# Kernel tuning notes

Hardware: AMD Instinct MI355X
Metric: run time of the kernel (lower is better)

The kernel has to match this reference:

```python
import jax, jax.numpy as jnp
import numpy as np

B, M, N, I, O, NM = 16, 256, 256, 64, 64, 16


def setup_inputs() -> dict:
    key = jax.random.key(0)
    k1, k2, k3, k4, k5 = jax.random.split(key, 5)
    glorot = 1.0 / np.sqrt(I + O)
    return {
        "x": jax.random.normal(k1, (B, M, N, I), dtype=jnp.float32),
        "fw1": jax.random.normal(k2, (I, O, NM, NM, 2), dtype=jnp.float32) * glorot,
        "fw2": jax.random.normal(k3, (I, O, NM, NM, 2), dtype=jnp.float32) * glorot,
        "W": jax.random.normal(k4, (I, O), dtype=jnp.float32) * glorot,
        "b": jnp.zeros((O,), dtype=jnp.float32),
    }


def reference(x, fw1, fw2, W, b):
    # x: [B, M, N, I] -> [B, I, M, N]
    Bs, Ms, Ns, Is = x.shape
    nm = fw1.shape[2]
    xt = jnp.transpose(x, (0, 3, 1, 2))
    # forward rFFT over spatial dims, scaled by 1/sqrt(M*N) as in the TF code
    x_ft = jnp.fft.rfft2(xt, s=(Ms, Ns))  # [B, I, M, N//2+1] complex64
    x_ft = x_ft / jnp.asarray(np.sqrt(Ms * Ns), dtype=x_ft.dtype)
    # complex weights (stack-of-2 real/imag -> complex); complex einsum is
    # exactly the real/imag stacked matmul in the original
    w1 = jax.lax.complex(fw1[..., 0], fw1[..., 1])
    w2 = jax.lax.complex(fw2[..., 0], fw2[..., 1])
    top = jnp.einsum('bixy,ioxy->boxy', x_ft[:, :, :nm, :nm], w1)
    bot = jnp.einsum('bixy,ioxy->boxy', x_ft[:, :, -nm:, :nm], w2)
    mid = jnp.zeros((Bs, top.shape[1], Ms - 2 * nm, nm), dtype=top.dtype)
    out_ft = jnp.concatenate([top, mid, bot], axis=2)          # [B, O, M, nm]
    pad = jnp.zeros((Bs, top.shape[1], Ms, Ms // 2 + 1 - nm), dtype=top.dtype)
    out_ft = jnp.concatenate([out_ft, pad], axis=3)            # [B, O, M, M//2+1]
    y = jnp.fft.irfft2(out_ft, s=(Ns, Ms))                     # [B, O, N, M]
    # TF rescale: sqrt(prod of last two dims of out_ft) = sqrt(N*(M//2+1))
    y = y * jnp.asarray(np.sqrt(Ns * (Ms // 2 + 1)), dtype=y.dtype)
    y = jnp.transpose(y, (0, 2, 3, 1))                         # [B, M, N, O]
    return jax.nn.relu(y @ W + b + y)
```

## Files before the change

kernel.cpp:

```cpp
#include <hip/hip_runtime.h>
#include <hip/hip_bf16.h>


#define PI2F 6.283185307179586f

typedef __attribute__((ext_vector_type(8))) short short8v;
typedef __attribute__((ext_vector_type(4))) float f32x4;

static __device__ __forceinline__ unsigned short f_to_bf16(float f) {
  unsigned int u = __float_as_uint(f);
  u += 0x7fffu + ((u >> 16) & 1u);
  return (unsigned short)(u >> 16);
}
static __device__ __forceinline__ unsigned int pack_bf16(float lo, float hi) {
  return (unsigned int)f_to_bf16(lo) | ((unsigned int)f_to_bf16(hi) << 16);
}

__global__ __launch_bounds__(256) void k_prep(const float* __restrict__ fw1,
                                              const float* __restrict__ fw2,
                                              float2* __restrict__ wT,
                                              unsigned short* __restrict__ Eg,
                                              unsigned short* __restrict__ CSg,
                                              const float* __restrict__ Wg,
                                              unsigned short* __restrict__ Wtb) {
  int t = threadIdx.x;
  if (blockIdx.x == 256) {
#pragma unroll
    for (int ky = 0; ky < 16; ++ky) {
      int idx = (ky * t) & 255;
      float ss, cc;
      sincosf(PI2F * (float)idx * (1.0f / 256.0f), &ss, &cc);
      Eg[(2 * ky) * 256 + t]     = f_to_bf16(cc);
      Eg[(2 * ky + 1) * 256 + t] = f_to_bf16(-ss);
      CSg[t * 32 + 2 * ky]       = f_to_bf16(cc);
      CSg[t * 32 + 2 * ky + 1]   = f_to_bf16(ss);
    }
#pragma unroll
    for (int k = 0; k < 16; ++k) {
      int p = k * 256 + t;
      Wtb[(p & 63) * 64 + (p >> 6)] = f_to_bf16(Wg[p]);
    }
    return;
  }
  int a  = blockIdx.x >> 3;
  int ic = blockIdx.x & 7;
  const float* w = (a < 16) ? fw1 : fw2;
  int xx = a & 15;
#pragma unroll
  for (int k = 0; k < 2; ++k) {
    int p = k * 256 + t;
    int i = ic * 8 + (p >> 6);
    int o = p & 63;
    const float4* s4 = reinterpret_cast<const float4*>(
        w + ((((size_t)i * 64 + o) * 16 + xx) * 16) * 2);
#pragma unroll
    for (int j = 0; j < 8; ++j) {
      float4 q = s4[j];
      wT[(((size_t)(2 * j) * 32 + a) * 64 + i) * 64 + o]     = make_float2(q.x, q.y);
      wT[(((size_t)(2 * j + 1) * 32 + a) * 64 + i) * 64 + o] = make_float2(q.z, q.w);
    }
  }
}

__global__ __launch_bounds__(256) void k1_mfma(const float* __restrict__ x,
                                               const unsigned short* __restrict__ Eg,
                                               unsigned int* __restrict__ Tb) {
  __shared__ __align__(16) unsigned short El[32 * 264];
  __shared__ __align__(16) float xs[2][2048];
  int bm = blockIdx.x;
  int b = bm >> 8, m = bm & 255;
  int tid = threadIdx.x;

  {
    const unsigned int* src = reinterpret_cast<const unsigned int*>(Eg);
    unsigned int* dst = reinterpret_cast<unsigned int*>(El);
#pragma unroll
    for (int t = 0; t < 16; ++t) {
      int idx = t * 256 + tid;
      dst[(idx >> 7) * 132 + (idx & 127)] = src[idx];
    }
  }

  const float* xrow = x + (size_t)bm * 16384;
  int lane = tid & 63, w = tid >> 6;
  int r16 = lane & 15, g4 = lane >> 4;

  {
    const float4* s = reinterpret_cast<const float4*>(xrow);
    float4 v0 = s[tid], v1 = s[256 + tid];
    float4* d = reinterpret_cast<float4*>(xs[0]);
    d[tid] = v0;
    d[256 + tid] = v1;
  }
  __syncthreads();

  f32x4 z = {0.f, 0.f, 0.f, 0.f};
  f32x4 acc0 = z, acc1 = z;

#pragma unroll
  for (int c = 0; c < 8; ++c) {
    int cur = c & 1;
    if (c < 7) {
      const float4* s = reinterpret_cast<const float4*>(xrow + (c + 1) * 2048);
      float4 v0 = s[tid], v1 = s[256 + tid];
      float4* d = reinterpret_cast<float4*>(xs[cur ^ 1]);
      d[tid] = v0;
      d[256 + tid] = v1;
    }
    const float* xb = &xs[cur][g4 * 8 * 64 + (w * 16 + r16)];
    float xv[8];
#pragma unroll
    for (int j = 0; j < 8; ++j) xv[j] = xb[j * 64];
    short8v bfr;
#pragma unroll
    for (int j = 0; j < 8; ++j) bfr[j] = (short)f_to_bf16(xv[j]);
    int nb = c * 32 + g4 * 8;
    short8v a0 = *reinterpret_cast<const short8v*>(&El[r16 * 264 + nb]);
    short8v a1 = *reinterpret_cast<const short8v*>(&El[(16 + r16) * 264 + nb]);
    acc0 = __builtin_amdgcn_mfma_f32_16x16x32_bf16(a0, bfr, acc0, 0, 0, 0);
    acc1 = __builtin_amdgcn_mfma_f32_16x16x32_bf16(a1, bfr, acc1, 0, 0, 0);
    __syncthreads();
  }

  const float SC = 1.0f / 256.0f;
  int i = w * 16 + r16;
#pragma unroll
  for (int mt = 0; mt < 2; ++mt) {
    f32x4 av = (mt == 0) ? acc0 : acc1;
    int ky_a = mt * 8 + g4 * 2;
    Tb[((size_t)(b * 16 + ky_a) * 256 + m) * 64 + i]     = pack_bf16(av[0] * SC, av[1] * SC);
    Tb[((size_t)(b * 16 + ky_a + 1) * 256 + m) * 64 + i] = pack_bf16(av[2] * SC, av[3] * SC);
  }
}

__global__ __launch_bounds__(256) void k2_fwd_m(const unsigned int* __restrict__ Tb,
                                                float* __restrict__ Xp) {
  int bx = blockIdx.x;
  int bky = bx & 255, mc = bx >> 8;
  int m0 = mc * 64;
  int ih = threadIdx.x & 15;
  int ag = threadIdx.x >> 4;
  const uint4* Tp4 = reinterpret_cast<const uint4*>(Tb) + (size_t)bky * 4096 + ih;

  float cd1, sd1n, cd2, sd2n;
  { float ss, cc; sincosf(PI2F * (float)ag * (1.0f / 256.0f), &ss, &cc); cd1 = cc; sd1n = -ss; }
  { float ss, cc; sincosf(PI2F * (float)(ag - 16) * (1.0f / 256.0f), &ss, &cc); cd2 = cc; sd2n = -ss; }
  float c1, s1, c2, s2;
  { int t = (ag * m0) & 255; float ss, cc; sincosf(PI2F * (float)t * (1.0f / 256.0f), &ss, &cc); c1 = cc; s1 = -ss; }
  { int t = ((ag + 240) * m0) & 255; float ss, cc; sincosf(PI2F * (float)t * (1.0f / 256.0f), &ss, &cc); c2 = cc; s2 = -ss; }

  float xr1[4], xi1[4], xr2[4], xi2[4];
#pragma unroll
  for (int ii = 0; ii < 4; ++ii) { xr1[ii] = xi1[ii] = xr2[ii] = xi2[ii] = 0.0f; }

#pragma unroll 4
  for (int m = 0; m < 64; ++m) {
    uint4 q = Tp4[(size_t)(m0 + m) * 16];
    unsigned int dv[4] = {q.x, q.y, q.z, q.w};
    float tre[4], tim[4];
#pragma unroll
    for (int ii = 0; ii < 4; ++ii) {
      tre[ii] = __uint_as_float(dv[ii] << 16);
      tim[ii] = __uint_as_float(dv[ii] & 0xffff0000u);
    }
#pragma unroll
    for (int ii = 0; ii < 4; ++ii) {
      xr1[ii] += tre[ii] * c1 - tim[ii] * s1;
      xi1[ii] += tre[ii] * s1 + tim[ii] * c1;
      xr2[ii] += tre[ii] * c2 - tim[ii] * s2;
      xi2[ii] += tre[ii] * s2 + tim[ii] * c2;
    }
    float cn;
    cn = c1 * cd1 - s1 * sd1n; s1 = c1 * sd1n + s1 * cd1; c1 = cn;
    cn = c2 * cd2 - s2 * sd2n; s2 = c2 * sd2n + s2 * cd2; c2 = cn;
  }

  float* Xb = Xp + (size_t)mc * 1048576;
  float* Xp1 = Xb + ((size_t)bky * 32 + ag) * 128 + ih * 8;
  float* Xp2 = Xb + ((size_t)bky * 32 + ag + 16) * 128 + ih * 8;
  reinterpret_cast<float4*>(Xp1)[0] = make_float4(xr1[0], xi1[0], xr1[1], xi1[1]);
  reinterpret_cast<float4*>(Xp1)[1] = make_float4(xr1[2], xi1[2], xr1[3], xi1[3]);
  reinterpret_cast<float4*>(Xp2)[0] = make_float4(xr2[0], xi2[0], xr2[1], xi2[1]);
  reinterpret_cast<float4*>(Xp2)[1] = make_float4(xr2[2], xi2[2], xr2[3], xi2[3]);
}

__global__ __launch_bounds__(256) void k3_mix(const float* __restrict__ Xp,
                                              const float* __restrict__ wT,
                                              float* __restrict__ OF) {
  int blk = blockIdx.x;
  int kyy = blk >> 5, a = blk & 31;
  __shared__ float wre[64 * 65];
  __shared__ float wim[64 * 65];
  __shared__ float xsh[16 * 128];

  const float2* wsrc = reinterpret_cast<const float2*>(wT) + (size_t)(kyy * 32 + a) * 4096;
#pragma unroll
  for (int k = 0; k < 16; ++k) {
    int p = k * 256 + (int)threadIdx.x;
    float2 v = wsrc[p];
    int i = p >> 6, o = p & 63;
    wre[i * 65 + o] = v.x;
    wim[i * 65 + o] = v.y;
  }
  {
    int bb = threadIdx.x >> 4, icn = threadIdx.x & 15;
    size_t off = ((size_t)(bb * 16 + kyy) * 32 + a) * 128;
    float4 a0 = make_float4(0.f, 0.f, 0.f, 0.f), a1 = a0;
#pragma unroll
    for (int c = 0; c < 4; ++c) {
      const float4* xsrc = reinterpret_cast<const float4*>(Xp + (size_t)c * 1048576 + off);
      float4 q0 = xsrc[icn * 2], q1 = xsrc[icn * 2 + 1];
      a0.x += q0.x; a0.y += q0.y; a0.z += q0.z; a0.w += q0.w;
      a1.x += q1.x; a1.y += q1.y; a1.z += q1.z; a1.w += q1.w;
    }
    float4* xdst = reinterpret_cast<float4*>(xsh + bb * 128);
    xdst[icn * 2]     = a0;
    xdst[icn * 2 + 1] = a1;
  }
  __syncthreads();

  int o = threadIdx.x & 63, bg = threadIdx.x >> 6;
#pragma unroll
  for (int bb = 0; bb < 4; ++bb) {
    int b = bg * 4 + bb;
    float ore = 0.0f, oim = 0.0f;
    for (int i = 0; i < 64; ++i) {
      float xr = xsh[b * 128 + 2 * i], xi = xsh[b * 128 + 2 * i + 1];
      float wr = wre[i * 65 + o],     wi = wim[i * 65 + o];
      ore += xr * wr - xi * wi;
      oim += xr * wi + xi * wr;
    }
    reinterpret_cast<float2*>(OF)[(((size_t)b * 16 + kyy) * 32 + a) * 64 + o] =
        make_float2(ore, oim);
  }
}

__global__ __launch_bounds__(256) void k4_inv_kx(const float* __restrict__ OF,
                                                 uint4* __restrict__ Gb4) {
  int bx = blockIdx.x;
  int b = bx >> 6, ug = (bx >> 2) & 15, chunk = bx & 3;
  __shared__ float ofs[16384];
  __shared__ float ct[256], st[256];
  {
    float ssv, ccv;
    sincosf(PI2F * (float)threadIdx.x * (1.0f / 256.0f), &ssv, &ccv);
    ct[threadIdx.x] = ccv;
    st[threadIdx.x] = ssv;
  }
  {
    const float4* src = reinterpret_cast<const float4*>(
        OF + ((size_t)b * 16 + chunk * 4) * 4096);
    float4* dst = reinterpret_cast<float4*>(ofs);
#pragma unroll
    for (int k = 0; k < 16; ++k) dst[k * 256 + threadIdx.x] = src[k * 256 + threadIdx.x];
  }
  __syncthreads();

  int o = threadIdx.x & 63, us = threadIdx.x >> 6;
  int u0 = ug * 16 + us * 4;
  const float SC2 = 0.002772904280510622f;

  float accr[4][4], acci[4][4];
#pragma unroll
  for (int du = 0; du < 4; ++du)
#pragma unroll
    for (int kyl = 0; kyl < 4; ++kyl) { accr[du][kyl] = 0.0f; acci[du][kyl] = 0.0f; }

  for (int a = 0; a < 32; ++a) {
    int kx = (a < 16) ? a : (224 + a);
    float ofr[4], ofi[4];
#pragma unroll
    for (int kyl = 0; kyl < 4; ++kyl) {
      ofr[kyl] = ofs[((kyl * 32 + a) * 64 + o) * 2];
      ofi[kyl] = ofs[((kyl * 32 + a) * 64 + o) * 2 + 1];
    }
#pragma unroll
    for (int du = 0; du < 4; ++du) {
      int t = (kx * (u0 + du)) & 255;
      float cv = ct[t], sv = st[t];
#pragma unroll
      for (int kyl = 0; kyl < 4; ++kyl) {
        accr[du][kyl] += ofr[kyl] * cv - ofi[kyl] * sv;
        acci[du][kyl] += ofr[kyl] * sv + ofi[kyl] * cv;
      }
    }
  }
#pragma unroll
  for (int du = 0; du < 4; ++du) {
    int u = u0 + du;
    unsigned int wv[4];
#pragma unroll
    for (int kyl = 0; kyl < 4; ++kyl) {
      int ky = chunk * 4 + kyl;
      float sc = SC2 * ((ky == 0) ? 1.0f : 2.0f);
      wv[kyl] = pack_bf16(accr[du][kyl] * sc, -acci[du][kyl] * sc);
    }
    uint4 pk; pk.x = wv[0]; pk.y = wv[1]; pk.z = wv[2]; pk.w = wv[3];
    Gb4[(((size_t)b * 256 + u) * 64 + o) * 4 + chunk] = pk;
  }
}

__global__ __launch_bounds__(256) void k5_mfma(const unsigned short* __restrict__ Gb,
                                               const unsigned short* __restrict__ CSg,
                                               const unsigned short* __restrict__ Wtb,
                                               const float* __restrict__ bias,
                                               float* __restrict__ out) {
  __shared__ __align__(16) unsigned short yl[256 * 72];

  int blk = blockIdx.x;
  int tid = threadIdx.x;
  int lane = tid & 63, w = tid >> 6;
  int r16 = lane & 15, g4 = lane >> 4;
  int kc0 = g4 * 8;

  f32x4 z = {0.f, 0.f, 0.f, 0.f};
  f32x4 acc[4][4];

  short8v af[4], bfx[4];
#pragma unroll
  for (int vt = 0; vt < 4; ++vt)
    af[vt] = *reinterpret_cast<const short8v*>(&CSg[(w * 64 + vt * 16 + r16) * 32 + kc0]);
#pragma unroll
  for (int ot = 0; ot < 4; ++ot)
    bfx[ot] = *reinterpret_cast<const short8v*>(
        &Gb[((size_t)blk * 64 + ot * 16 + r16) * 32 + kc0]);
#pragma unroll
  for (int vt = 0; vt < 4; ++vt)
#pragma unroll
    for (int ot = 0; ot < 4; ++ot)
      acc[vt][ot] = __builtin_amdgcn_mfma_f32_16x16x32_bf16(af[vt], bfx[ot], z, 0, 0, 0);

#pragma unroll
  for (int vt = 0; vt < 4; ++vt)
#pragma unroll
    for (int ot = 0; ot < 4; ++ot)
#pragma unroll
      for (int r = 0; r < 4; ++r)
        yl[(w * 64 + vt * 16 + g4 * 4 + r) * 72 + ot * 16 + r16] = f_to_bf16(acc[vt][ot][r]);

#pragma unroll
  for (int ot = 0; ot < 4; ++ot) {
    float bv = bias[ot * 16 + r16];
#pragma unroll
    for (int vt = 0; vt < 4; ++vt)
#pragma unroll
      for (int r = 0; r < 4; ++r) acc[vt][ot][r] += bv;
  }

#pragma unroll
  for (int ks = 0; ks < 2; ++ks) {
    int k0 = ks * 32 + kc0;
    short8v ya[4], wb[4];
#pragma unroll
    for (int vt = 0; vt < 4; ++vt)
      ya[vt] = *reinterpret_cast<const short8v*>(&yl[(w * 64 + vt * 16 + r16) * 72 + k0]);
#pragma unroll
    for (int ot = 0; ot < 4; ++ot)
      wb[ot] = *reinterpret_cast<const short8v*>(&Wtb[(ot * 16 + r16) * 64 + k0]);
#pragma unroll
    for (int vt = 0; vt < 4; ++vt)
#pragma unroll
      for (int ot = 0; ot < 4; ++ot)
        acc[vt][ot] = __builtin_amdgcn_mfma_f32_16x16x32_bf16(ya[vt], wb[ot], acc[vt][ot], 0, 0, 0);
  }

  float* ob = out + (size_t)blk * 16384;
  float* tw = reinterpret_cast<float*>(&yl[w * 4608]);
#pragma unroll
  for (int vt = 0; vt < 4; ++vt) {
#pragma unroll
    for (int ot = 0; ot < 4; ++ot)
#pragma unroll
      for (int r = 0; r < 4; ++r)
        tw[(g4 * 4 + r) * 68 + ot * 16 + r16] = fmaxf(acc[vt][ot][r], 0.0f);
    float* obase = ob + (size_t)(w * 64 + vt * 16) * 64;
#pragma unroll
    for (int q = 0; q < 4; ++q) {
      float4 vv = *reinterpret_cast<const float4*>(
          &tw[(q * 4 + (lane >> 4)) * 68 + (lane & 15) * 4]);
      *reinterpret_cast<float4*>(&obase[q * 256 + lane * 4]) = vv;
    }
  }
}

extern "C" void kernel_launch(void* const* d_in, const int* in_sizes, int n_in,
                              void* d_out, int out_size, void* d_ws, size_t ws_size,
                              hipStream_t stream) {
  const float* x   = (const float*)d_in[0];
  const float* fw1 = (const float*)d_in[1];
  const float* fw2 = (const float*)d_in[2];
  const float* W   = (const float*)d_in[3];
  const float* bb  = (const float*)d_in[4];
  float* out = (float*)d_out;

  float* ws = (float*)d_ws;
  float* wT          = ws;
  unsigned int* Tb   = (unsigned int*)(ws + 4194304);
  float* Xp          = ws + 8388608;
  float* OF          = ws + 12582912;
  unsigned int* Gb   = (unsigned int*)(ws + 13631488);
  unsigned short* Eg  = (unsigned short*)(ws + 17825792);
  unsigned short* CSg = Eg + 8192;
  unsigned short* Wtb = CSg + 8192;

  hipLaunchKernelGGL(k_prep,   dim3(257),  dim3(256), 0, stream,
                     fw1, fw2, (float2*)wT, Eg, CSg, W, Wtb);
  hipLaunchKernelGGL(k1_mfma,  dim3(4096), dim3(256), 0, stream, x, Eg, Tb);
  hipLaunchKernelGGL(k2_fwd_m, dim3(1024), dim3(256), 0, stream, Tb, Xp);
  hipLaunchKernelGGL(k3_mix,   dim3(512),  dim3(256), 0, stream, Xp, wT, OF);
  hipLaunchKernelGGL(k4_inv_kx,dim3(1024), dim3(256), 0, stream, OF, (uint4*)Gb);
  hipLaunchKernelGGL(k5_mfma,  dim3(4096), dim3(256), 0, stream,
                     (const unsigned short*)Gb, CSg, Wtb, bb, out);
}
```

Baseline: 233.6 us.

## Read spectral weights directly in mixing kernel and split inverse kx work finer

The weight transpose pass in the prep kernel is removed, so the mixing kernel now gathers complex weights straight from fw1/fw2 with strided float2 loads, and the prep kernel shrinks to a single block for twiddle and W tables. This drops a 16 MB write and re-read of a transposed weight copy, at the cost of uncoalesced 8-byte reads (stride 128 bytes) in the mixing kernel. Separately, the inverse-kx kernel now processes 2 ky values per block instead of 4, doubling the grid to 2048 blocks and halving shared memory per block for better occupancy. It writes 8-byte packed pairs instead of 16-byte ones.

```diff
diff --git a/kernel.cpp b/kernel.cpp
--- a/kernel.cpp
+++ b/kernel.cpp
@@ -16,49 +16,25 @@
   return (unsigned int)f_to_bf16(lo) | ((unsigned int)f_to_bf16(hi) << 16);
 }
 
-__global__ __launch_bounds__(256) void k_prep(const float* __restrict__ fw1,
-                                              const float* __restrict__ fw2,
-                                              float2* __restrict__ wT,
-                                              unsigned short* __restrict__ Eg,
-                                              unsigned short* __restrict__ CSg,
-                                              const float* __restrict__ Wg,
-                                              unsigned short* __restrict__ Wtb) {
+__global__ __launch_bounds__(256) void k_prep1(unsigned short* __restrict__ Eg,
+                                               unsigned short* __restrict__ CSg,
+                                               const float* __restrict__ Wg,
+                                               unsigned short* __restrict__ Wtb) {
   int t = threadIdx.x;
-  if (blockIdx.x == 256) {
-#pragma unroll
-    for (int ky = 0; ky < 16; ++ky) {
-      int idx = (ky * t) & 255;
-      float ss, cc;
-      sincosf(PI2F * (float)idx * (1.0f / 256.0f), &ss, &cc);
-      Eg[(2 * ky) * 256 + t]     = f_to_bf16(cc);
-      Eg[(2 * ky + 1) * 256 + t] = f_to_bf16(-ss);
-      CSg[t * 32 + 2 * ky]       = f_to_bf16(cc);
-      CSg[t * 32 + 2 * ky + 1]   = f_to_bf16(ss);
-    }
-#pragma unroll
-    for (int k = 0; k < 16; ++k) {
-      int p = k * 256 + t;
-      Wtb[(p & 63) * 64 + (p >> 6)] = f_to_bf16(Wg[p]);
-    }
-    return;
-  }
-  int a  = blockIdx.x >> 3;
-  int ic = blockIdx.x & 7;
-  const float* w = (a < 16) ? fw1 : fw2;
-  int xx = a & 15;
-#pragma unroll
-  for (int k = 0; k < 2; ++k) {
+#pragma unroll
+  for (int ky = 0; ky < 16; ++ky) {
+    int idx = (ky * t) & 255;
+    float ss, cc;
+    sincosf(PI2F * (float)idx * (1.0f / 256.0f), &ss, &cc);
+    Eg[(2 * ky) * 256 + t]     = f_to_bf16(cc);
+    Eg[(2 * ky + 1) * 256 + t] = f_to_bf16(-ss);
+    CSg[t * 32 + 2 * ky]       = f_to_bf16(cc);
+    CSg[t * 32 + 2 * ky + 1]   = f_to_bf16(ss);
+  }
+#pragma unroll
+  for (int k = 0; k < 16; ++k) {
     int p = k * 256 + t;
-    int i = ic * 8 + (p >> 6);
-    int o = p & 63;
-    const float4* s4 = reinterpret_cast<const float4*>(
-        w + ((((size_t)i * 64 + o) * 16 + xx) * 16) * 2);
-#pragma unroll
-    for (int j = 0; j < 8; ++j) {
-      float4 q = s4[j];
-      wT[(((size_t)(2 * j) * 32 + a) * 64 + i) * 64 + o]     = make_float2(q.x, q.y);
-      wT[(((size_t)(2 * j + 1) * 32 + a) * 64 + i) * 64 + o] = make_float2(q.z, q.w);
-    }
+    Wtb[(p & 63) * 64 + (p >> 6)] = f_to_bf16(Wg[p]);
   }
 }
 
@@ -185,7 +161,8 @@
 }
 
 __global__ __launch_bounds__(256) void k3_mix(const float* __restrict__ Xp,
-                                              const float* __restrict__ wT,
+                                              const float* __restrict__ fw1,
+                                              const float* __restrict__ fw2,
                                               float* __restrict__ OF) {
   int blk = blockIdx.x;
   int kyy = blk >> 5, a = blk & 31;
@@ -193,11 +170,12 @@
   __shared__ float wim[64 * 65];
   __shared__ float xsh[16 * 128];
 
-  const float2* wsrc = reinterpret_cast<const float2*>(wT) + (size_t)(kyy * 32 + a) * 4096;
+  const float* w = (a < 16) ? fw1 : fw2;
+  int xx = a & 15;
 #pragma unroll
   for (int k = 0; k < 16; ++k) {
     int p = k * 256 + (int)threadIdx.x;
-    float2 v = wsrc[p];
+    float2 v = *reinterpret_cast<const float2*>(w + ((size_t)p * 16 + xx) * 32 + kyy * 2);
     int i = p >> 6, o = p & 63;
     wre[i * 65 + o] = v.x;
     wim[i * 65 + o] = v.y;
@@ -236,10 +214,10 @@
 }
 
 __global__ __launch_bounds__(256) void k4_inv_kx(const float* __restrict__ OF,
-                                                 uint4* __restrict__ Gb4) {
+                                                 unsigned int* __restrict__ Gbd) {
   int bx = blockIdx.x;
-  int b = bx >> 6, ug = (bx >> 2) & 15, chunk = bx & 3;
-  __shared__ float ofs[16384];
+  int b = bx >> 7, ug = (bx >> 3) & 15, kyc = bx & 7;
+  __shared__ float ofs[8192];
   __shared__ float ct[256], st[256];
   {
     float ssv, ccv;
@@ -249,10 +227,10 @@
   }
   {
     const float4* src = reinterpret_cast<const float4*>(
-        OF + ((size_t)b * 16 + chunk * 4) * 4096);
+        OF + ((size_t)b * 16 + kyc * 2) * 4096);
     float4* dst = reinterpret_cast<float4*>(ofs);
 #pragma unroll
-    for (int k = 0; k < 16; ++k) dst[k * 256 + threadIdx.x] = src[k * 256 + threadIdx.x];
+    for (int k = 0; k < 8; ++k) dst[k * 256 + threadIdx.x] = src[k * 256 + threadIdx.x];
   }
   __syncthreads();
 
@@ -260,17 +238,17 @@
   int u0 = ug * 16 + us * 4;
   const float SC2 = 0.002772904280510622f;
 
-  float accr[4][4], acci[4][4];
+  float accr[4][2], acci[4][2];
 #pragma unroll
   for (int du = 0; du < 4; ++du)
 #pragma unroll
-    for (int kyl = 0; kyl < 4; ++kyl) { accr[du][kyl] = 0.0f; acci[du][kyl] = 0.0f; }
+    for (int kyl = 0; kyl < 2; ++kyl) { accr[du][kyl] = 0.0f; acci[du][kyl] = 0.0f; }
 
   for (int a = 0; a < 32; ++a) {
     int kx = (a < 16) ? a : (224 + a);
-    float ofr[4], ofi[4];
-#pragma unroll
-    for (int kyl = 0; kyl < 4; ++kyl) {
+    float ofr[2], ofi[2];
+#pragma unroll
+    for (int kyl = 0; kyl < 2; ++kyl) {
       ofr[kyl] = ofs[((kyl * 32 + a) * 64 + o) * 2];
       ofi[kyl] = ofs[((kyl * 32 + a) * 64 + o) * 2 + 1];
     }
@@ -279,7 +257,7 @@
       int t = (kx * (u0 + du)) & 255;
       float cv = ct[t], sv = st[t];
 #pragma unroll
-      for (int kyl = 0; kyl < 4; ++kyl) {
+      for (int kyl = 0; kyl < 2; ++kyl) {
         accr[du][kyl] += ofr[kyl] * cv - ofi[kyl] * sv;
         acci[du][kyl] += ofr[kyl] * sv + ofi[kyl] * cv;
       }
@@ -288,15 +266,16 @@
 #pragma unroll
   for (int du = 0; du < 4; ++du) {
     int u = u0 + du;
-    unsigned int wv[4];
-#pragma unroll
-    for (int kyl = 0; kyl < 4; ++kyl) {
-      int ky = chunk * 4 + kyl;
+    unsigned int wv[2];
+#pragma unroll
+    for (int kyl = 0; kyl < 2; ++kyl) {
+      int ky = kyc * 2 + kyl;
       float sc = SC2 * ((ky == 0) ? 1.0f : 2.0f);
       wv[kyl] = pack_bf16(accr[du][kyl] * sc, -acci[du][kyl] * sc);
     }
-    uint4 pk; pk.x = wv[0]; pk.y = wv[1]; pk.z = wv[2]; pk.w = wv[3];
-    Gb4[(((size_t)b * 256 + u) * 64 + o) * 4 + chunk] = pk;
+    uint2 pk; pk.x = wv[0]; pk.y = wv[1];
+    *reinterpret_cast<uint2*>(
+        &Gbd[(((size_t)b * 256 + u) * 64 + o) * 16 + kyc * 2]) = pk;
   }
 }
 
@@ -394,7 +373,6 @@
   float* out = (float*)d_out;
 
   float* ws = (float*)d_ws;
-  float* wT          = ws;
   unsigned int* Tb   = (unsigned int*)(ws + 4194304);
   float* Xp          = ws + 8388608;
   float* OF          = ws + 12582912;
@@ -403,12 +381,11 @@
   unsigned short* CSg = Eg + 8192;
   unsigned short* Wtb = CSg + 8192;
 
-  hipLaunchKernelGGL(k_prep,   dim3(257),  dim3(256), 0, stream,
-                     fw1, fw2, (float2*)wT, Eg, CSg, W, Wtb);
+  hipLaunchKernelGGL(k_prep1,  dim3(1),    dim3(256), 0, stream, Eg, CSg, W, Wtb);
   hipLaunchKernelGGL(k1_mfma,  dim3(4096), dim3(256), 0, stream, x, Eg, Tb);
   hipLaunchKernelGGL(k2_fwd_m, dim3(1024), dim3(256), 0, stream, Tb, Xp);
-  hipLaunchKernelGGL(k3_mix,   dim3(512),  dim3(256), 0, stream, Xp, wT, OF);
-  hipLaunchKernelGGL(k4_inv_kx,dim3(1024), dim3(256), 0, stream, OF, (uint4*)Gb);
+  hipLaunchKernelGGL(k3_mix,   dim3(512),  dim3(256), 0, stream, Xp, fw1, fw2, OF);
+  hipLaunchKernelGGL(k4_inv_kx,dim3(2048), dim3(256), 0, stream, OF, Gb);
   hipLaunchKernelGGL(k5_mfma,  dim3(4096), dim3(256), 0, stream,
                      (const unsigned short*)Gb, CSg, Wtb, bb, out);
 }
```

Result: slower. 241.7 us (+3.5%).

## Swizzle x staging in LDS, fold forward scale into twiddles, restructure Gb layout

Applied to the files above, without the earlier changes.

The first kernel now stores x tiles into shared memory with an XOR swizzle so the column-strided reads feeding the MFMA avoid bank conflicts. The 1/256 scale moves from the per-output multiply into the precomputed bf16 twiddle table. k4 drops its 64KB shared-memory staging of OF and reads float2 values directly from global memory, which should raise occupancy but relies on cache for reuse. The Gb intermediate is transposed to a chunk-major layout so k4's stores coalesce across o, and k5's loads are changed to match.

```diff
diff --git a/kernel.cpp b/kernel.cpp
--- a/kernel.cpp
+++ b/kernel.cpp
@@ -25,13 +25,14 @@
                                               unsigned short* __restrict__ Wtb) {
   int t = threadIdx.x;
   if (blockIdx.x == 256) {
+    const float SC = 1.0f / 256.0f;
 #pragma unroll
     for (int ky = 0; ky < 16; ++ky) {
       int idx = (ky * t) & 255;
       float ss, cc;
       sincosf(PI2F * (float)idx * (1.0f / 256.0f), &ss, &cc);
-      Eg[(2 * ky) * 256 + t]     = f_to_bf16(cc);
-      Eg[(2 * ky + 1) * 256 + t] = f_to_bf16(-ss);
+      Eg[(2 * ky) * 256 + t]     = f_to_bf16(cc * SC);
+      Eg[(2 * ky + 1) * 256 + t] = f_to_bf16(-ss * SC);
       CSg[t * 32 + 2 * ky]       = f_to_bf16(cc);
       CSg[t * 32 + 2 * ky + 1]   = f_to_bf16(ss);
     }
@@ -85,12 +86,18 @@
   int lane = tid & 63, w = tid >> 6;
   int r16 = lane & 15, g4 = lane >> 4;
 
+  int r0 = tid >> 4;
+  int c4 = (tid & 15) * 4;
+  int off0 = r0 * 64 + (c4 ^ (((r0 >> 3) & 3) << 4));
+  int r1 = 16 + r0;
+  int off1 = r1 * 64 + (c4 ^ (((r1 >> 3) & 3) << 4));
+  int colr = (w * 16 + r16) ^ (g4 << 4);
+
   {
     const float4* s = reinterpret_cast<const float4*>(xrow);
     float4 v0 = s[tid], v1 = s[256 + tid];
-    float4* d = reinterpret_cast<float4*>(xs[0]);
-    d[tid] = v0;
-    d[256 + tid] = v1;
+    *reinterpret_cast<float4*>(&xs[0][off0]) = v0;
+    *reinterpret_cast<float4*>(&xs[0][off1]) = v1;
   }
   __syncthreads();
 
@@ -103,11 +110,10 @@
     if (c < 7) {
       const float4* s = reinterpret_cast<const float4*>(xrow + (c + 1) * 2048);
       float4 v0 = s[tid], v1 = s[256 + tid];
-      float4* d = reinterpret_cast<float4*>(xs[cur ^ 1]);
-      d[tid] = v0;
-      d[256 + tid] = v1;
-    }
-    const float* xb = &xs[cur][g4 * 8 * 64 + (w * 16 + r16)];
+      *reinterpret_cast<float4*>(&xs[cur ^ 1][off0]) = v0;
+      *reinterpret_cast<float4*>(&xs[cur ^ 1][off1]) = v1;
+    }
+    const float* xb = &xs[cur][g4 * 8 * 64 + colr];
     float xv[8];
 #pragma unroll
     for (int j = 0; j < 8; ++j) xv[j] = xb[j * 64];
@@ -122,14 +128,13 @@
     __syncthreads();
   }
 
-  const float SC = 1.0f / 256.0f;
   int i = w * 16 + r16;
 #pragma unroll
   for (int mt = 0; mt < 2; ++mt) {
     f32x4 av = (mt == 0) ? acc0 : acc1;
     int ky_a = mt * 8 + g4 * 2;
-    Tb[((size_t)(b * 16 + ky_a) * 256 + m) * 64 + i]     = pack_bf16(av[0] * SC, av[1] * SC);
-    Tb[((size_t)(b * 16 + ky_a + 1) * 256 + m) * 64 + i] = pack_bf16(av[2] * SC, av[3] * SC);
+    Tb[((size_t)(b * 16 + ky_a) * 256 + m) * 64 + i]     = pack_bf16(av[0], av[1]);
+    Tb[((size_t)(b * 16 + ky_a + 1) * 256 + m) * 64 + i] = pack_bf16(av[2], av[3]);
   }
 }
 
@@ -239,7 +244,6 @@
                                                  uint4* __restrict__ Gb4) {
   int bx = blockIdx.x;
   int b = bx >> 6, ug = (bx >> 2) & 15, chunk = bx & 3;
-  __shared__ float ofs[16384];
   __shared__ float ct[256], st[256];
   {
     float ssv, ccv;
@@ -247,18 +251,13 @@
     ct[threadIdx.x] = ccv;
     st[threadIdx.x] = ssv;
   }
-  {
-    const float4* src = reinterpret_cast<const float4*>(
-        OF + ((size_t)b * 16 + chunk * 4) * 4096);
-    float4* dst = reinterpret_cast<float4*>(ofs);
-#pragma unroll
-    for (int k = 0; k < 16; ++k) dst[k * 256 + threadIdx.x] = src[k * 256 + threadIdx.x];
-  }
   __syncthreads();
 
   int o = threadIdx.x & 63, us = threadIdx.x >> 6;
   int u0 = ug * 16 + us * 4;
   const float SC2 = 0.002772904280510622f;
+  const float2* OFb = reinterpret_cast<const float2*>(OF) +
+                      ((size_t)b * 16 + chunk * 4) * 2048;
 
   float accr[4][4], acci[4][4];
 #pragma unroll
@@ -271,8 +270,8 @@
     float ofr[4], ofi[4];
 #pragma unroll
     for (int kyl = 0; kyl < 4; ++kyl) {
-      ofr[kyl] = ofs[((kyl * 32 + a) * 64 + o) * 2];
-      ofi[kyl] = ofs[((kyl * 32 + a) * 64 + o) * 2 + 1];
+      float2 v = OFb[(kyl * 32 + a) * 64 + o];
+      ofr[kyl] = v.x; ofi[kyl] = v.y;
     }
 #pragma unroll
     for (int du = 0; du < 4; ++du) {
@@ -296,7 +295,7 @@
       wv[kyl] = pack_bf16(accr[du][kyl] * sc, -acci[du][kyl] * sc);
     }
     uint4 pk; pk.x = wv[0]; pk.y = wv[1]; pk.z = wv[2]; pk.w = wv[3];
-    Gb4[(((size_t)b * 256 + u) * 64 + o) * 4 + chunk] = pk;
+    Gb4[(((size_t)b * 256 + u) * 4 + chunk) * 64 + o] = pk;
   }
 }
 
@@ -323,7 +322,7 @@
 #pragma unroll
   for (int ot = 0; ot < 4; ++ot)
     bfx[ot] = *reinterpret_cast<const short8v*>(
-        &Gb[((size_t)blk * 64 + ot * 16 + r16) * 32 + kc0]);
+        &Gb[(((size_t)blk * 4 + g4) * 64 + ot * 16 + r16) * 8]);
 #pragma unroll
   for (int vt = 0; vt < 4; ++vt)
 #pragma unroll
```

New measurement: 234.6 us. No clear change (+0.4%).
